# Kernel optimization log

Hardware: AMD Instinct MI355X
Metric: run time of the kernel (lower is better)

The kernel has to match this reference:

```python
import jax, jax.numpy as jnp
import numpy as np

TEMPERATURE = 0.07


def _unit(k, shape):
    x = jax.random.normal(k, shape, dtype=jnp.float32)
    return x / jnp.linalg.norm(x, axis=-1, keepdims=True)


def setup_inputs() -> dict:
    key = jax.random.key(0)
    ks = jax.random.split(key, 7)
    B, Cml, Cmc, D = 8192, 2048, 1000, 512
    features = _unit(ks[0], (B, D))
    ml_text = _unit(ks[1], (Cml, D))
    mc_text = _unit(ks[2], (Cmc, D))
    multilabel_targets = (jax.random.uniform(ks[3], (B, Cml)) < 0.05).astype(jnp.float32)
    # one-hot multiclass targets
    mc_idx = jax.random.randint(ks[4], (B,), 0, Cmc)
    multiclass_targets = jax.nn.one_hot(mc_idx, Cmc, dtype=jnp.float32)
    dataset_indices = jax.random.randint(ks[5], (B,), 0, 2).astype(jnp.int32)
    ratios = jax.random.uniform(ks[6], (Cml,), minval=0.05, maxval=0.95, dtype=jnp.float32)
    return {
        "features": features,
        "multilabel_text_features": ml_text,
        "multiclass_text_features": mc_text,
        "multilabel_targets": multilabel_targets,
        "multiclass_targets": multiclass_targets,
        "dataset_indices": dataset_indices,
        "ratios": ratios,
    }


def iterate_M(sim_matrix, b, num_iterations=2):
    # sim_matrix: [B, C, 2]; b: [C, 2]
    P = jnp.exp(sim_matrix)
    for _ in range(num_iterations):
        P = P / P.sum(axis=2, keepdims=True)          # row (last-dim) normalize
        P = P / (P.sum(axis=0) / b)                   # column normalize to marginals b
    return P


def iterate_P(sim_matrix, m, num_iterations=5):
    # sim_matrix: [B, C]
    P = jnp.exp(sim_matrix)
    for _ in range(num_iterations):
        row_sums = P.sum(axis=1)
        P = P / jnp.maximum(row_sums, 1.0)[:, None]
        P = P * m / P.sum()
    return P


def reference(features, multilabel_text_features, multiclass_text_features,
              multilabel_targets, multiclass_targets, dataset_indices, ratios):
    ml_sim = features @ multilabel_text_features.T / TEMPERATURE   # [B, Cml]
    mc_sim = features @ multiclass_text_features.T / TEMPERATURE   # [B, Cmc]

    n_mc = jnp.sum(dataset_indices == 1).astype(jnp.float32)
    n_ml = jnp.sum(dataset_indices == 0).astype(jnp.float32)
    m = n_mc + n_ml * 0.1

    P = iterate_P(mc_sim, m, 5)

    bs = ml_sim.shape[0]
    sim3 = jnp.stack([ml_sim / 2, -ml_sim / 2], axis=-1)           # [B, Cml, 2]
    b = jnp.stack([ratios, 1.0 - ratios], axis=1) * bs             # [Cml, 2]
    M = iterate_M(sim3, b, 2)

    ml_targets_final = jnp.stack([multilabel_targets, 1.0 - multilabel_targets], axis=-1)
    multilabel_loss = -jnp.sum(ml_targets_final * jnp.log(M)) * 0.5
    multiclass_loss = -jnp.sum(multiclass_targets * jnp.log(P))
    total_loss = multiclass_loss + multilabel_loss
    return total_loss
```

## Files before the change

kernel.cpp:

```cpp
#include <hip/hip_runtime.h>

typedef unsigned short u16;
typedef float f32x4 __attribute__((ext_vector_type(4)));
typedef short s16x8 __attribute__((ext_vector_type(8)));

#define GPTR(x) ((const __attribute__((address_space(1))) void*)(x))
#define LPTR(x) ((__attribute__((address_space(3))) void*)(x))

__device__ __forceinline__ u16 f32_to_bf16(float f) {
  unsigned u = __builtin_bit_cast(unsigned, f);
  u += 0x7FFFu + ((u >> 16) & 1u);
  return (u16)(u >> 16);
}
__device__ __forceinline__ float bf16_to_f32(u16 h) {
  unsigned u = ((unsigned)h) << 16;
  return __builtin_bit_cast(float, u);
}

__global__ __launch_bounds__(256) void k_cvt_all(
    const float* __restrict__ A, const float* __restrict__ ML, const float* __restrict__ MC,
    u16* __restrict__ Abf, u16* __restrict__ Bbf)
{
  int i = blockIdx.x * 256 + threadIdx.x;
  const float* src; u16* dst; int idx;
  bool pad = false;
  if (i < 1048576) { src = A; dst = Abf; idx = i; }
  else {
    int j = i - 1048576;
    if (j >= 393216) return;
    int row = j >> 7;
    dst = Bbf; idx = j;
    if (row < 2048) { src = ML; }
    else {
      int mcrow = row - 2048;
      src = MC; idx = j - 2048 * 128;
      pad = (mcrow >= 1000);
    }
  }
  ushort4 o = {0, 0, 0, 0};
  if (!pad) {
    float4 v = reinterpret_cast<const float4*>(src)[idx];
    o.x = f32_to_bf16(v.x); o.y = f32_to_bf16(v.y);
    o.z = f32_to_bf16(v.z); o.w = f32_to_bf16(v.w);
  }
  reinterpret_cast<ushort4*>(dst)[idx] = o;
}

__global__ __launch_bounds__(512, 1) void k_gemm_fused(
    const u16* __restrict__ A, const u16* __restrict__ Bg,
    u16* __restrict__ Sml, float* __restrict__ colpart, float* __restrict__ pexp,
    float scale)
{
  constexpr int BK = 64;
  __shared__ __align__(16) u16 As[3][256 * BK];
  __shared__ __align__(16) u16 Bs[3][128 * BK];
  __shared__ float sredf[512];

  const int tid  = threadIdx.x;
  const int lane = tid & 63;
  const int wave = tid >> 6;
  const int wr = wave >> 1;
  const int wc = wave & 1;

  int wg = (blockIdx.x & 7) * 96 + (blockIdx.x >> 3);
  const int bm = wg / 24;
  const int bn = wg % 24;
  const int row0 = bm * 256;
  const int col0 = bn * 128;
  const bool is_ml = (bn < 16);

  const int cr = (lane >> 4) * 4;
  const int cc = lane & 15;

  if (tid < 128) sredf[tid] = 0.f;

  f32x4 acc[4][4];
#pragma unroll
  for (int i = 0; i < 4; ++i)
#pragma unroll
    for (int j = 0; j < 4; ++j) acc[i][j] = (f32x4){0.f, 0.f, 0.f, 0.f};

  auto stage = [&](int buf, int k0) {
#pragma unroll
    for (int q = 0; q < 4; ++q) {
      int base = wave * 256 + q * 64;
      int slot = base + lane;
      int r = slot >> 3, s = slot & 7;
      int sg = s ^ (r & 7);
      __builtin_amdgcn_global_load_lds(GPTR(A + (size_t)(row0 + r) * 512 + k0 + sg * 8),
                                       LPTR(&As[buf][base * 8]), 16, 0, 0);
    }
#pragma unroll
    for (int q = 0; q < 2; ++q) {
      int base = wave * 128 + q * 64;
      int slot = base + lane;
      int r = slot >> 3, s = slot & 7;
      int sg = s ^ (r & 7);
      __builtin_amdgcn_global_load_lds(GPTR(Bg + (size_t)(col0 + r) * 512 + k0 + sg * 8),
                                       LPTR(&Bs[buf][base * 8]), 16, 0, 0);
    }
  };

  stage(0, 0);
  stage(1, BK);
#pragma unroll
  for (int t = 0; t < 8; ++t) {
    const int cur = t % 3;
    if (t < 7) { asm volatile("s_waitcnt vmcnt(6)" ::: "memory"); }
    else       { asm volatile("s_waitcnt vmcnt(0)" ::: "memory"); }
    __builtin_amdgcn_sched_barrier(0);
    __builtin_amdgcn_s_barrier();
    asm volatile("" ::: "memory");
    __builtin_amdgcn_sched_barrier(0);
    if (t + 2 < 8) stage((t + 2) % 3, (t + 2) * BK);
#pragma unroll
    for (int ks = 0; ks < 2; ++ks) {
      s16x8 af[4], bf[4];
#pragma unroll
      for (int mm = 0; mm < 4; ++mm) {
        int r = wr * 64 + mm * 16 + (lane & 15);
        int ss = (ks * 4 + (lane >> 4)) ^ (r & 7);
        af[mm] = *reinterpret_cast<const s16x8*>(&As[cur][r * BK + ss * 8]);
      }
#pragma unroll
      for (int nn = 0; nn < 4; ++nn) {
        int r = wc * 64 + nn * 16 + (lane & 15);
        int ss = (ks * 4 + (lane >> 4)) ^ (r & 7);
        bf[nn] = *reinterpret_cast<const s16x8*>(&Bs[cur][r * BK + ss * 8]);
      }
      __builtin_amdgcn_s_setprio(1);
#pragma unroll
      for (int mm = 0; mm < 4; ++mm)
#pragma unroll
        for (int nn = 0; nn < 4; ++nn)
          acc[mm][nn] = __builtin_amdgcn_mfma_f32_16x16x32_bf16(af[mm], bf[nn], acc[mm][nn], 0, 0, 0);
      __builtin_amdgcn_s_setprio(0);
    }
  }

  if (is_ml) {
#pragma unroll
    for (int mm = 0; mm < 4; ++mm) {
      int orow = row0 + wr * 64 + mm * 16 + cr;
#pragma unroll
      for (int nn = 0; nn < 4; ++nn) {
        int ocol = col0 + wc * 64 + nn * 16 + cc;
#pragma unroll
        for (int r = 0; r < 4; ++r)
          Sml[(size_t)(orow + r) * 2048 + ocol] = f32_to_bf16(acc[mm][nn][r] * scale);
      }
    }
#pragma unroll
    for (int nn = 0; nn < 4; ++nn) {
      float cs = 0.f;
#pragma unroll
      for (int mm = 0; mm < 4; ++mm)
#pragma unroll
        for (int r = 0; r < 4; ++r) {
          float s = acc[mm][nn][r] * scale;
          cs += 1.f / (1.f + __expf(-s));
        }
      cs += __shfl_xor(cs, 16);
      cs += __shfl_xor(cs, 32);
      if (lane < 16) atomicAdd(&sredf[wc * 64 + nn * 16 + lane], cs);
    }
    __syncthreads();
    if (tid < 128) colpart[(size_t)bm * 2048 + col0 + tid] = sredf[tid];
  } else {
    const int mccol0 = col0 - 2048;
    float ex[16];
#pragma unroll
    for (int mm = 0; mm < 4; ++mm)
#pragma unroll
      for (int r = 0; r < 4; ++r) {
        float e = 0.f;
#pragma unroll
        for (int nn = 0; nn < 4; ++nn) {
          int ocol = mccol0 + wc * 64 + nn * 16 + cc;
          float s = acc[mm][nn][r] * scale;
          if (ocol < 1000) e += __expf(s);
        }
        ex[mm * 4 + r] = e;
      }
#pragma unroll
    for (int o = 1; o < 16; o <<= 1)
#pragma unroll
      for (int q = 0; q < 16; ++q) ex[q] += __shfl_xor(ex[q], o);
    __syncthreads();
    if ((lane & 15) == 0) {
#pragma unroll
      for (int mm = 0; mm < 4; ++mm)
#pragma unroll
        for (int r = 0; r < 4; ++r) {
          int lrow = wr * 64 + mm * 16 + cr + r;
          sredf[lrow * 2 + wc] = ex[mm * 4 + r];
        }
    }
    __syncthreads();
    if (tid < 256) {
      size_t o = (size_t)(bn - 16) * 8192 + row0 + tid;
      pexp[o] = sredf[tid * 2] + sredf[tid * 2 + 1];
    }
  }
}

__global__ void k_reduce_c(const float* __restrict__ part, const float* __restrict__ ratios,
                           float* __restrict__ c) {
  int j = blockIdx.x * 256 + threadIdx.x;
  float s = 0.f;
  for (int ch = 0; ch < 32; ++ch) s += part[ch * 2048 + j];
  float b0 = ratios[j] * 8192.f;
  float b1 = (1.f - ratios[j]) * 8192.f;
  c[2 * j]     = b0 / s;
  c[2 * j + 1] = b1 / (8192.f - s);
}

__global__ __launch_bounds__(256) void k_ml_pass2(
    const u16* __restrict__ S, const float* __restrict__ T, const float* __restrict__ c,
    float* __restrict__ part2, float* __restrict__ partT, float* __restrict__ partE)
{
  const int t = threadIdx.x;
  const int r0 = blockIdx.x * 8;
  float c0[8], c1[8];
#pragma unroll
  for (int q = 0; q < 4; ++q) {
    float4 cv = reinterpret_cast<const float4*>(c)[t * 4 + q];
    c0[q * 2]     = cv.x; c1[q * 2]     = cv.y;
    c0[q * 2 + 1] = cv.z; c1[q * 2 + 1] = cv.w;
  }

  float q0s[8], ts[8];
#pragma unroll
  for (int k = 0; k < 8; ++k) { q0s[k] = 0.f; ts[k] = 0.f; }
  float tss = 0.f, ldsum = 0.f;

#pragma unroll 2
  for (int r = 0; r < 8; ++r) {
    size_t row = r0 + r;
    s16x8 sv = *reinterpret_cast<const s16x8*>(S + row * 2048 + t * 8);
    float4 ta = reinterpret_cast<const float4*>(T + row * 2048)[t * 2];
    float4 tb = reinterpret_cast<const float4*>(T + row * 2048)[t * 2 + 1];
    float tv[8] = {ta.x, ta.y, ta.z, ta.w, tb.x, tb.y, tb.z, tb.w};
#pragma unroll
    for (int k = 0; k < 8; ++k) {
      float s = bf16_to_f32((u16)sv[k]);
      float e = __expf(s);
      float n0 = e * c0[k];
      float den = n0 + c1[k];
      q0s[k] += n0 * __builtin_amdgcn_rcpf(den);
      ldsum  += __logf(den);
      ts[k]  += tv[k];
      tss    += tv[k] * s;
    }
  }
  float es = tss - ldsum;
#pragma unroll
  for (int k = 0; k < 8; ++k)
    es += __logf(c0[k] / c1[k]) * ts[k] + 8.f * __logf(c1[k]);

  float* p2 = part2 + (size_t)blockIdx.x * 2048 + t * 8;
  float* pT = partT + (size_t)blockIdx.x * 2048 + t * 8;
#pragma unroll
  for (int q = 0; q < 2; ++q) {
    reinterpret_cast<float4*>(p2)[q] = (float4){q0s[q*4], q0s[q*4+1], q0s[q*4+2], q0s[q*4+3]};
    reinterpret_cast<float4*>(pT)[q] = (float4){ts[q*4], ts[q*4+1], ts[q*4+2], ts[q*4+3]};
  }

  __shared__ float red[256];
  red[t] = es;
  __syncthreads();
  for (int o = 128; o; o >>= 1) {
    if (t < o) red[t] += red[t + o];
    __syncthreads();
  }
  if (t == 0) partE[blockIdx.x] = red[0];
}

__global__ __launch_bounds__(256) void k_colredA(
    const float* __restrict__ part2, const float* __restrict__ partT,
    float* __restrict__ pA2, float* __restrict__ pAT)
{
  int j = blockIdx.x * 256 + threadIdx.x;
  int ch0 = blockIdx.y * 16;
  float cs2 = 0.f, Tj = 0.f;
  for (int ch = ch0; ch < ch0 + 16; ++ch) {
    cs2 += part2[(size_t)ch * 2048 + j];
    Tj  += partT[(size_t)ch * 2048 + j];
  }
  pA2[(size_t)blockIdx.y * 2048 + j] = cs2;
  pAT[(size_t)blockIdx.y * 2048 + j] = Tj;
}

__global__ __launch_bounds__(256) void k_colredB(
    const float* __restrict__ pA2, const float* __restrict__ pAT,
    const float* __restrict__ ratios, float* __restrict__ partCol)
{
  int j = blockIdx.x * 256 + threadIdx.x;
  float cs2 = 0.f, Tj = 0.f;
  for (int ch = 0; ch < 64; ++ch) {
    cs2 += pA2[(size_t)ch * 2048 + j];
    Tj  += pAT[(size_t)ch * 2048 + j];
  }
  float b0 = ratios[j] * 8192.f;
  float b1 = (1.f - ratios[j]) * 8192.f;
  float colp = Tj * __logf(b0 / cs2) + (8192.f - Tj) * __logf(b1 / (8192.f - cs2));
  __shared__ float red[256];
  red[threadIdx.x] = colp;
  __syncthreads();
  for (int o = 128; o; o >>= 1) {
    if (threadIdx.x < o) red[threadIdx.x] += red[threadIdx.x + o];
    __syncthreads();
  }
  if (threadIdx.x == 0) partCol[blockIdx.x] = red[0];
}

__global__ __launch_bounds__(256) void k_mc_rowdot(
    const float* __restrict__ T2, const u16* __restrict__ A, const u16* __restrict__ B,
    float* __restrict__ rowdot, float scale)
{
  int wave = threadIdx.x >> 6, lane = threadIdx.x & 63;
  int row = blockIdx.x * 4 + wave;
  const float4* t4 = reinterpret_cast<const float4*>(T2 + (size_t)row * 1000);
  int idx = -1;
#pragma unroll
  for (int g = 0; g < 4; ++g) {
    int j4 = lane + g * 64;
    if (j4 < 250) {
      float4 v = t4[j4];
      if (v.x > 0.5f) idx = j4 * 4;
      if (v.y > 0.5f) idx = j4 * 4 + 1;
      if (v.z > 0.5f) idx = j4 * 4 + 2;
      if (v.w > 0.5f) idx = j4 * 4 + 3;
    }
  }
#pragma unroll
  for (int o = 32; o; o >>= 1) idx = max(idx, __shfl_xor(idx, o));

  s16x8 va = *reinterpret_cast<const s16x8*>(A + (size_t)row * 512 + lane * 8);
  s16x8 vb = *reinterpret_cast<const s16x8*>(B + (size_t)(2048 + idx) * 512 + lane * 8);
  float d = 0.f;
#pragma unroll
  for (int k = 0; k < 8; ++k)
    d += bf16_to_f32((u16)va[k]) * bf16_to_f32((u16)vb[k]);
#pragma unroll
  for (int o = 32; o; o >>= 1) d += __shfl_xor(d, o);
  if (lane == 0) rowdot[row] = d * scale;
}

__global__ __launch_bounds__(1024) void k_finalize(
    const float* __restrict__ pexp, const float* __restrict__ rowdot,
    const int* __restrict__ ds,
    const float* __restrict__ partE, const float* __restrict__ partCol,
    float* __restrict__ out)
{
  __shared__ float red[1024];
  const int tid = threadIdx.x;

  auto bsum = [&](float v) -> float {
    __syncthreads();
    red[tid] = v;
    __syncthreads();
    for (int o = 512; o; o >>= 1) {
      if (tid < o) red[tid] += red[tid + o];
      __syncthreads();
    }
    return red[0];
  };

  float nmc = 0.f, nml = 0.f;
  for (int i = tid; i < 8192; i += 1024) {
    int d = ds[i];
    nmc += (d == 1) ? 1.f : 0.f;
    nml += (d == 0) ? 1.f : 0.f;
  }
  float n_mc = bsum(nmc);
  float n_ml = bsum(nml);
  float m = n_mc + 0.1f * n_ml;

  float a[8], Rv[8], rdv[8];
#pragma unroll
  for (int q = 0; q < 8; ++q) {
    int i = tid + q * 1024;
    float e = 0.f;
#pragma unroll
    for (int ch = 0; ch < 8; ++ch) e += pexp[(size_t)ch * 8192 + i];
    Rv[q] = e; rdv[q] = rowdot[i]; a[q] = 1.f;
  }
  for (int it = 0; it < 5; ++it) {
    float p = 0.f;
#pragma unroll
    for (int q = 0; q < 8; ++q) {
      a[q] = a[q] / fmaxf(Rv[q] * a[q], 1.f);
      p += Rv[q] * a[q];
    }
    float tot = bsum(p);
    float sc = m / tot;
#pragma unroll
    for (int q = 0; q < 8; ++q) a[q] *= sc;
  }
  float mcp = 0.f;
#pragma unroll
  for (int q = 0; q < 8; ++q)
    mcp += rdv[q] + __logf(a[q]);

  float ep = partE[tid];
  float cp = 0.f;
  if (tid < 8) cp = partCol[tid];

  float total = bsum(-mcp - 0.5f * (cp + ep));
  if (tid == 0) out[0] = total;
}

extern "C" void kernel_launch(void* const* d_in, const int* in_sizes, int n_in,
                              void* d_out, int out_size, void* d_ws, size_t ws_size,
                              hipStream_t stream)
{
  const float* features = (const float*)d_in[0];
  const float* ml_text  = (const float*)d_in[1];
  const float* mc_text  = (const float*)d_in[2];
  const float* ml_tgt   = (const float*)d_in[3];
  const float* mc_tgt   = (const float*)d_in[4];
  const int*   dsidx    = (const int*)d_in[5];
  const float* ratios   = (const float*)d_in[6];
  float* out = (float*)d_out;

  char* ws = (char*)d_ws;
  size_t off = 0;
  auto alloc = [&](size_t bytes) -> void* {
    void* p = ws + off;
    off += (bytes + 255) & ~(size_t)255;
    return p;
  };
  u16*   Abf    = (u16*)alloc((size_t)8192 * 512 * 2);
  u16*   Bbf    = (u16*)alloc((size_t)3072 * 512 * 2);
  u16*   Sml    = (u16*)alloc((size_t)8192 * 2048 * 2);
  float* part1  = (float*)alloc((size_t)32 * 2048 * 4);
  float* cbuf   = (float*)alloc((size_t)2048 * 2 * 4);
  float* part2  = (float*)alloc((size_t)1024 * 2048 * 4);
  float* partT  = (float*)alloc((size_t)1024 * 2048 * 4);
  float* pA2    = (float*)alloc((size_t)64 * 2048 * 4);
  float* pAT    = (float*)alloc((size_t)64 * 2048 * 4);
  float* partE  = (float*)alloc((size_t)1024 * 4);
  float* partCol= (float*)alloc((size_t)8 * 4);
  float* pexp   = (float*)alloc((size_t)8 * 8192 * 4);
  float* rowdot = (float*)alloc((size_t)8192 * 4);

  k_cvt_all<<<(1441792 + 255) / 256, 256, 0, stream>>>(features, ml_text, mc_text, Abf, Bbf);

  const float scale = 1.0f / 0.07f;
  k_gemm_fused<<<768, 512, 0, stream>>>(Abf, Bbf, Sml, part1, pexp, scale);

  k_mc_rowdot<<<2048, 256, 0, stream>>>(mc_tgt, Abf, Bbf, rowdot, scale);
  k_reduce_c<<<8, 256, 0, stream>>>(part1, ratios, cbuf);
  k_ml_pass2<<<1024, 256, 0, stream>>>(Sml, ml_tgt, cbuf, part2, partT, partE);
  k_colredA<<<dim3(8, 64), 256, 0, stream>>>(part2, partT, pA2, pAT);
  k_colredB<<<8, 256, 0, stream>>>(pA2, pAT, ratios, partCol);
  k_finalize<<<1, 1024, 0, stream>>>(pexp, rowdot, dsidx, partE, partCol, out);
}
```

Baseline: 122.4 us.

## Shrink GEMM tile to 128x128 single-buffered and merge small reduction kernels

The fused GEMM goes from 256x128 tiles with 512 threads and a triple-buffered async LDS pipeline to 128x128 tiles with 256 threads, one LDS buffer and plain syncthreads, so twice as many blocks are launched. The column-partial buffer doubles to 64 chunks to match. The reduce_c and mc_rowdot kernels are merged into one launch, and colredB is folded into the single-block finalize kernel. This cuts launch count and raises occupancy, but it drops the load/compute overlap and per-tile data reuse, and finalize now does more serial work in one block.

```diff
diff --git a/kernel.cpp b/kernel.cpp
--- a/kernel.cpp
+++ b/kernel.cpp
@@ -46,15 +46,16 @@
   reinterpret_cast<ushort4*>(dst)[idx] = o;
 }
 
-__global__ __launch_bounds__(512, 1) void k_gemm_fused(
+__global__ __launch_bounds__(256) void k_gemm_fused(
     const u16* __restrict__ A, const u16* __restrict__ Bg,
     u16* __restrict__ Sml, float* __restrict__ colpart, float* __restrict__ pexp,
     float scale)
 {
+  constexpr int K = 512;
   constexpr int BK = 64;
-  __shared__ __align__(16) u16 As[3][256 * BK];
-  __shared__ __align__(16) u16 Bs[3][128 * BK];
-  __shared__ float sredf[512];
+  __shared__ __align__(16) u16 As[128 * BK];
+  __shared__ __align__(16) u16 Bs[128 * BK];
+  __shared__ float sredf[256];
 
   const int tid  = threadIdx.x;
   const int lane = tid & 63;
@@ -62,57 +63,36 @@
   const int wr = wave >> 1;
   const int wc = wave & 1;
 
-  int wg = (blockIdx.x & 7) * 96 + (blockIdx.x >> 3);
+  int wg = (blockIdx.x & 7) * 192 + (blockIdx.x >> 3);
   const int bm = wg / 24;
   const int bn = wg % 24;
-  const int row0 = bm * 256;
+  const int row0 = bm * 128;
   const int col0 = bn * 128;
   const bool is_ml = (bn < 16);
 
   const int cr = (lane >> 4) * 4;
   const int cc = lane & 15;
 
-  if (tid < 128) sredf[tid] = 0.f;
-
   f32x4 acc[4][4];
 #pragma unroll
   for (int i = 0; i < 4; ++i)
 #pragma unroll
     for (int j = 0; j < 4; ++j) acc[i][j] = (f32x4){0.f, 0.f, 0.f, 0.f};
 
-  auto stage = [&](int buf, int k0) {
+  for (int k0 = 0; k0 < K; k0 += BK) {
+    __syncthreads();
 #pragma unroll
     for (int q = 0; q < 4; ++q) {
       int base = wave * 256 + q * 64;
       int slot = base + lane;
       int r = slot >> 3, s = slot & 7;
       int sg = s ^ (r & 7);
-      __builtin_amdgcn_global_load_lds(GPTR(A + (size_t)(row0 + r) * 512 + k0 + sg * 8),
-                                       LPTR(&As[buf][base * 8]), 16, 0, 0);
-    }
-#pragma unroll
-    for (int q = 0; q < 2; ++q) {
-      int base = wave * 128 + q * 64;
-      int slot = base + lane;
-      int r = slot >> 3, s = slot & 7;
-      int sg = s ^ (r & 7);
-      __builtin_amdgcn_global_load_lds(GPTR(Bg + (size_t)(col0 + r) * 512 + k0 + sg * 8),
-                                       LPTR(&Bs[buf][base * 8]), 16, 0, 0);
-    }
-  };
-
-  stage(0, 0);
-  stage(1, BK);
-#pragma unroll
-  for (int t = 0; t < 8; ++t) {
-    const int cur = t % 3;
-    if (t < 7) { asm volatile("s_waitcnt vmcnt(6)" ::: "memory"); }
-    else       { asm volatile("s_waitcnt vmcnt(0)" ::: "memory"); }
-    __builtin_amdgcn_sched_barrier(0);
-    __builtin_amdgcn_s_barrier();
-    asm volatile("" ::: "memory");
-    __builtin_amdgcn_sched_barrier(0);
-    if (t + 2 < 8) stage((t + 2) % 3, (t + 2) * BK);
+      __builtin_amdgcn_global_load_lds(GPTR(A + (size_t)(row0 + r) * K + k0 + sg * 8),
+                                       LPTR(&As[base * 8]), 16, 0, 0);
+      __builtin_amdgcn_global_load_lds(GPTR(Bg + (size_t)(col0 + r) * K + k0 + sg * 8),
+                                       LPTR(&Bs[base * 8]), 16, 0, 0);
+    }
+    __syncthreads();
 #pragma unroll
     for (int ks = 0; ks < 2; ++ks) {
       s16x8 af[4], bf[4];
@@ -120,21 +100,19 @@
       for (int mm = 0; mm < 4; ++mm) {
         int r = wr * 64 + mm * 16 + (lane & 15);
         int ss = (ks * 4 + (lane >> 4)) ^ (r & 7);
-        af[mm] = *reinterpret_cast<const s16x8*>(&As[cur][r * BK + ss * 8]);
+        af[mm] = *reinterpret_cast<const s16x8*>(&As[r * BK + ss * 8]);
       }
 #pragma unroll
       for (int nn = 0; nn < 4; ++nn) {
         int r = wc * 64 + nn * 16 + (lane & 15);
         int ss = (ks * 4 + (lane >> 4)) ^ (r & 7);
-        bf[nn] = *reinterpret_cast<const s16x8*>(&Bs[cur][r * BK + ss * 8]);
+        bf[nn] = *reinterpret_cast<const s16x8*>(&Bs[r * BK + ss * 8]);
       }
-      __builtin_amdgcn_s_setprio(1);
 #pragma unroll
       for (int mm = 0; mm < 4; ++mm)
 #pragma unroll
         for (int nn = 0; nn < 4; ++nn)
           acc[mm][nn] = __builtin_amdgcn_mfma_f32_16x16x32_bf16(af[mm], bf[nn], acc[mm][nn], 0, 0, 0);
-      __builtin_amdgcn_s_setprio(0);
     }
   }
 
@@ -150,6 +128,8 @@
           Sml[(size_t)(orow + r) * 2048 + ocol] = f32_to_bf16(acc[mm][nn][r] * scale);
       }
     }
+    if (tid < 128) sredf[tid] = 0.f;
+    __syncthreads();
 #pragma unroll
     for (int nn = 0; nn < 4; ++nn) {
       float cs = 0.f;
@@ -197,22 +177,55 @@
         }
     }
     __syncthreads();
-    if (tid < 256) {
+    if (tid < 128) {
       size_t o = (size_t)(bn - 16) * 8192 + row0 + tid;
       pexp[o] = sredf[tid * 2] + sredf[tid * 2 + 1];
     }
   }
 }
 
-__global__ void k_reduce_c(const float* __restrict__ part, const float* __restrict__ ratios,
-                           float* __restrict__ c) {
-  int j = blockIdx.x * 256 + threadIdx.x;
-  float s = 0.f;
-  for (int ch = 0; ch < 32; ++ch) s += part[ch * 2048 + j];
-  float b0 = ratios[j] * 8192.f;
-  float b1 = (1.f - ratios[j]) * 8192.f;
-  c[2 * j]     = b0 / s;
-  c[2 * j + 1] = b1 / (8192.f - s);
+__global__ __launch_bounds__(256) void k_misc(
+    const float* __restrict__ part, const float* __restrict__ ratios, float* __restrict__ c,
+    const float* __restrict__ T2, const u16* __restrict__ A, const u16* __restrict__ B,
+    float* __restrict__ rowdot, float scale)
+{
+  if (blockIdx.x < 8) {
+    int j = blockIdx.x * 256 + threadIdx.x;
+    float s = 0.f;
+    for (int ch = 0; ch < 64; ++ch) s += part[ch * 2048 + j];
+    float b0 = ratios[j] * 8192.f;
+    float b1 = (1.f - ratios[j]) * 8192.f;
+    c[2 * j]     = b0 / s;
+    c[2 * j + 1] = b1 / (8192.f - s);
+    return;
+  }
+  int wave = threadIdx.x >> 6, lane = threadIdx.x & 63;
+  int row = (blockIdx.x - 8) * 4 + wave;
+  const float4* t4 = reinterpret_cast<const float4*>(T2 + (size_t)row * 1000);
+  int idx = -1;
+#pragma unroll
+  for (int g = 0; g < 4; ++g) {
+    int j4 = lane + g * 64;
+    if (j4 < 250) {
+      float4 v = t4[j4];
+      if (v.x > 0.5f) idx = j4 * 4;
+      if (v.y > 0.5f) idx = j4 * 4 + 1;
+      if (v.z > 0.5f) idx = j4 * 4 + 2;
+      if (v.w > 0.5f) idx = j4 * 4 + 3;
+    }
+  }
+#pragma unroll
+  for (int o = 32; o; o >>= 1) idx = max(idx, __shfl_xor(idx, o));
+
+  s16x8 va = *reinterpret_cast<const s16x8*>(A + (size_t)row * 512 + lane * 8);
+  s16x8 vb = *reinterpret_cast<const s16x8*>(B + (size_t)(2048 + idx) * 512 + lane * 8);
+  float d = 0.f;
+#pragma unroll
+  for (int k = 0; k < 8; ++k)
+    d += bf16_to_f32((u16)va[k]) * bf16_to_f32((u16)vb[k]);
+#pragma unroll
+  for (int o = 32; o; o >>= 1) d += __shfl_xor(d, o);
+  if (lane == 0) rowdot[row] = d * scale;
 }
 
 __global__ __launch_bounds__(256) void k_ml_pass2(
@@ -291,67 +304,11 @@
   pAT[(size_t)blockIdx.y * 2048 + j] = Tj;
 }
 
-__global__ __launch_bounds__(256) void k_colredB(
-    const float* __restrict__ pA2, const float* __restrict__ pAT,
-    const float* __restrict__ ratios, float* __restrict__ partCol)
-{
-  int j = blockIdx.x * 256 + threadIdx.x;
-  float cs2 = 0.f, Tj = 0.f;
-  for (int ch = 0; ch < 64; ++ch) {
-    cs2 += pA2[(size_t)ch * 2048 + j];
-    Tj  += pAT[(size_t)ch * 2048 + j];
-  }
-  float b0 = ratios[j] * 8192.f;
-  float b1 = (1.f - ratios[j]) * 8192.f;
-  float colp = Tj * __logf(b0 / cs2) + (8192.f - Tj) * __logf(b1 / (8192.f - cs2));
-  __shared__ float red[256];
-  red[threadIdx.x] = colp;
-  __syncthreads();
-  for (int o = 128; o; o >>= 1) {
-    if (threadIdx.x < o) red[threadIdx.x] += red[threadIdx.x + o];
-    __syncthreads();
-  }
-  if (threadIdx.x == 0) partCol[blockIdx.x] = red[0];
-}
-
-__global__ __launch_bounds__(256) void k_mc_rowdot(
-    const float* __restrict__ T2, const u16* __restrict__ A, const u16* __restrict__ B,
-    float* __restrict__ rowdot, float scale)
-{
-  int wave = threadIdx.x >> 6, lane = threadIdx.x & 63;
-  int row = blockIdx.x * 4 + wave;
-  const float4* t4 = reinterpret_cast<const float4*>(T2 + (size_t)row * 1000);
-  int idx = -1;
-#pragma unroll
-  for (int g = 0; g < 4; ++g) {
-    int j4 = lane + g * 64;
-    if (j4 < 250) {
-      float4 v = t4[j4];
-      if (v.x > 0.5f) idx = j4 * 4;
-      if (v.y > 0.5f) idx = j4 * 4 + 1;
-      if (v.z > 0.5f) idx = j4 * 4 + 2;
-      if (v.w > 0.5f) idx = j4 * 4 + 3;
-    }
-  }
-#pragma unroll
-  for (int o = 32; o; o >>= 1) idx = max(idx, __shfl_xor(idx, o));
-
-  s16x8 va = *reinterpret_cast<const s16x8*>(A + (size_t)row * 512 + lane * 8);
-  s16x8 vb = *reinterpret_cast<const s16x8*>(B + (size_t)(2048 + idx) * 512 + lane * 8);
-  float d = 0.f;
-#pragma unroll
-  for (int k = 0; k < 8; ++k)
-    d += bf16_to_f32((u16)va[k]) * bf16_to_f32((u16)vb[k]);
-#pragma unroll
-  for (int o = 32; o; o >>= 1) d += __shfl_xor(d, o);
-  if (lane == 0) rowdot[row] = d * scale;
-}
-
 __global__ __launch_bounds__(1024) void k_finalize(
     const float* __restrict__ pexp, const float* __restrict__ rowdot,
-    const int* __restrict__ ds,
-    const float* __restrict__ partE, const float* __restrict__ partCol,
-    float* __restrict__ out)
+    const int* __restrict__ ds, const float* __restrict__ partE,
+    const float* __restrict__ pA2, const float* __restrict__ pAT,
+    const float* __restrict__ ratios, float* __restrict__ out)
 {
   __shared__ float red[1024];
   const int tid = threadIdx.x;
@@ -403,9 +360,21 @@
   for (int q = 0; q < 8; ++q)
     mcp += rdv[q] + __logf(a[q]);
 
+  float cp = 0.f;
+#pragma unroll
+  for (int u = 0; u < 2; ++u) {
+    int j = tid * 2 + u;
+    float cs2 = 0.f, Tj = 0.f;
+    for (int ch = 0; ch < 64; ++ch) {
+      cs2 += pA2[(size_t)ch * 2048 + j];
+      Tj  += pAT[(size_t)ch * 2048 + j];
+    }
+    float b0 = ratios[j] * 8192.f;
+    float b1 = (1.f - ratios[j]) * 8192.f;
+    cp += Tj * __logf(b0 / cs2) + (8192.f - Tj) * __logf(b1 / (8192.f - cs2));
+  }
+
   float ep = partE[tid];
-  float cp = 0.f;
-  if (tid < 8) cp = partCol[tid];
 
   float total = bsum(-mcp - 0.5f * (cp + ep));
   if (tid == 0) out[0] = total;
@@ -434,26 +403,23 @@
   u16*   Abf    = (u16*)alloc((size_t)8192 * 512 * 2);
   u16*   Bbf    = (u16*)alloc((size_t)3072 * 512 * 2);
   u16*   Sml    = (u16*)alloc((size_t)8192 * 2048 * 2);
-  float* part1  = (float*)alloc((size_t)32 * 2048 * 4);
+  float* part1  = (float*)alloc((size_t)64 * 2048 * 4);
   float* cbuf   = (float*)alloc((size_t)2048 * 2 * 4);
   float* part2  = (float*)alloc((size_t)1024 * 2048 * 4);
   float* partT  = (float*)alloc((size_t)1024 * 2048 * 4);
   float* pA2    = (float*)alloc((size_t)64 * 2048 * 4);
   float* pAT    = (float*)alloc((size_t)64 * 2048 * 4);
   float* partE  = (float*)alloc((size_t)1024 * 4);
-  float* partCol= (float*)alloc((size_t)8 * 4);
   float* pexp   = (float*)alloc((size_t)8 * 8192 * 4);
   float* rowdot = (float*)alloc((size_t)8192 * 4);
 
   k_cvt_all<<<(1441792 + 255) / 256, 256, 0, stream>>>(features, ml_text, mc_text, Abf, Bbf);
 
   const float scale = 1.0f / 0.07f;
-  k_gemm_fused<<<768, 512, 0, stream>>>(Abf, Bbf, Sml, part1, pexp, scale);
-
-  k_mc_rowdot<<<2048, 256, 0, stream>>>(mc_tgt, Abf, Bbf, rowdot, scale);
-  k_reduce_c<<<8, 256, 0, stream>>>(part1, ratios, cbuf);
+  k_gemm_fused<<<1536, 256, 0, stream>>>(Abf, Bbf, Sml, part1, pexp, scale);
+
+  k_misc<<<8 + 2048, 256, 0, stream>>>(part1, ratios, cbuf, mc_tgt, Abf, Bbf, rowdot, scale);
   k_ml_pass2<<<1024, 256, 0, stream>>>(Sml, ml_tgt, cbuf, part2, partT, partE);
   k_colredA<<<dim3(8, 64), 256, 0, stream>>>(part2, partT, pA2, pAT);
-  k_colredB<<<8, 256, 0, stream>>>(pA2, pAT, ratios, partCol);
-  k_finalize<<<1, 1024, 0, stream>>>(pexp, rowdot, dsidx, partE, partCol, out);
-}
+  k_finalize<<<1, 1024, 0, stream>>>(pexp, rowdot, dsidx, partE, pA2, pAT, ratios, out);
+}
```

Result: slower. 135.9 us (+11.0%).
